# Optimization experiments

Hardware: AMD Instinct MI355X
Metric: run time of the kernel (lower is better)

The kernel has to match this reference:

```python
import jax, jax.numpy as jnp
import numpy as np

DIM = 512
NUM_HEADS = 8
HEAD_DIM = DIM // NUM_HEADS
FFN_DIM = 4 * DIM
EPS = 1e-6


def rmsnorm(x, w):
    rms = jnp.sqrt(jnp.mean(x * x, axis=-1, keepdims=True) + EPS)
    return x / rms * w


def setup_inputs() -> dict:
    key = jax.random.key(0)
    ks = jax.random.split(key, 8)
    B, T = 4, 2048
    x = jax.random.normal(ks[0], (B, T, DIM), dtype=jnp.float32)
    # Linear weights stored as [in, out] (transpose of torch layout)
    w_qkv = jax.random.normal(ks[1], (DIM, 3 * DIM), dtype=jnp.float32) * 0.02
    w_out = jax.random.normal(ks[2], (DIM, DIM), dtype=jnp.float32) * 0.02
    b_out = jnp.zeros((DIM,), dtype=jnp.float32)
    w1 = jax.random.normal(ks[3], (DIM, FFN_DIM), dtype=jnp.float32) * 0.02
    b1 = jnp.zeros((FFN_DIM,), dtype=jnp.float32)
    w2 = jax.random.normal(ks[4], (FFN_DIM, DIM), dtype=jnp.float32) * 0.02
    b2 = jnp.zeros((DIM,), dtype=jnp.float32)
    norm1_w = jnp.ones((DIM,), dtype=jnp.float32)
    norm2_w = jnp.ones((DIM,), dtype=jnp.float32)
    return {
        "x": x, "norm1_w": norm1_w, "norm2_w": norm2_w,
        "w_qkv": w_qkv, "w_out": w_out, "b_out": b_out,
        "w1": w1, "b1": b1, "w2": w2, "b2": b2,
        "context_size": 64,
    }


def reference(x, norm1_w, norm2_w, w_qkv, w_out, b_out, w1, b1, w2, b2, context_size):
    B, T, D = x.shape
    H, Hd = NUM_HEADS, HEAD_DIM
    # --- attention sublayer ---
    xn = rmsnorm(x, norm1_w)
    qkv = xn @ w_qkv                      # (B, T, 3D)
    q, k, v = jnp.split(qkv, 3, axis=-1)
    q = q.reshape(B, T, H, Hd).transpose(0, 2, 1, 3)  # (B, H, T, Hd)
    k = k.reshape(B, T, H, Hd).transpose(0, 2, 1, 3)
    v = v.reshape(B, T, H, Hd).transpose(0, 2, 1, 3)
    scale = Hd ** -0.5
    scores = jnp.einsum('bhqd,bhkd->bhqk', q, k) * scale  # (B, H, T, T)
    idx = jnp.arange(T)
    band = jnp.abs(idx[:, None] - idx[None, :]) <= context_size  # (T, T)
    scores = jnp.where(band[None, None], scores, -jnp.inf)
    attn = jax.nn.softmax(scores, axis=-1)
    out = jnp.einsum('bhqk,bhkd->bhqd', attn, v)  # (B, H, T, Hd)
    out = out.transpose(0, 2, 1, 3).reshape(B, T, D)
    out = out @ w_out + b_out
    x = x + out
    # --- FFN sublayer ---
    h = rmsnorm(x, norm2_w)
    h = jax.nn.gelu(h @ w1 + b1, approximate=False)
    x = x + (h @ w2 + b2)
    return x
```

## Files before the change

### kernel.cpp

```cpp
#include <hip/hip_runtime.h>
#include <cstdint>
#include <cstddef>

#define B_  4
#define T_  2048
#define D_  512
#define NH_ 8
#define HD_ 64
#define FF_ 2048
#define M_  (B_*T_)

typedef unsigned short u16;
typedef __attribute__((ext_vector_type(8))) unsigned short u16x8;
typedef __attribute__((ext_vector_type(8))) __bf16         bf16x8;
typedef __attribute__((ext_vector_type(4))) float          f32x4;

__device__ __forceinline__ u16 f2bf(float f) {
  unsigned u = __float_as_uint(f);
  u += 0x7FFF + ((u >> 16) & 1);
  return (u16)(u >> 16);
}
__device__ __forceinline__ float bf2f(u16 h) {
  return __uint_as_float((unsigned)h << 16);
}

__device__ __forceinline__ f32x4 mfma_bf16(u16x8 a, u16x8 b, f32x4 c) {
  return __builtin_amdgcn_mfma_f32_16x16x32_bf16(
      __builtin_bit_cast(bf16x8, a), __builtin_bit_cast(bf16x8, b), c, 0, 0, 0);
}

__device__ __forceinline__ void async16(const void* g, void* l) {
  __builtin_amdgcn_global_load_lds(
      (const __attribute__((address_space(1))) unsigned int*)g,
      (__attribute__((address_space(3))) unsigned int*)l, 16, 0, 0);
}

__device__ __forceinline__ float gelu_f(float v) {
  float ax = fabsf(v) * 0.70710678118f;
  float t = 1.0f / (1.0f + 0.3275911f * ax);
  float p = ((((1.061405429f * t - 1.453152027f) * t + 1.421413741f) * t
              - 0.284496736f) * t + 0.254829592f) * t;
  float e = __expf(-ax * ax);
  float er = 1.0f - p * e;
  float s = (v >= 0.0f) ? er : -er;
  return 0.5f * v * (1.0f + s);
}

__global__ __launch_bounds__(256) void prep_kernel(
    const float* __restrict__ i0, u16* __restrict__ o0,
    const float* __restrict__ i1, u16* __restrict__ o1,
    const float* __restrict__ i2, u16* __restrict__ o2,
    const float* __restrict__ i3, u16* __restrict__ o3,
    const float* __restrict__ x, const float* __restrict__ n1w,
    const float* __restrict__ n2w,
    float* __restrict__ inv, u16* __restrict__ xbf, float* __restrict__ ssz) {
  __shared__ float tile[32][33];
  const int bid = blockIdx.x, tid = threadIdx.x;
  if (bid < 3072) {
    const float* in; u16* out; const float* sc; int R, C, gx, lb;
    if (bid < 768)       { in = i0; out = o0; R = 512;  C = 1536; gx = 48; lb = bid;        sc = n1w; }
    else if (bid < 1024) { in = i1; out = o1; R = 512;  C = 512;  gx = 16; lb = bid - 768;  sc = nullptr; }
    else if (bid < 2048) { in = i2; out = o2; R = 512;  C = 2048; gx = 64; lb = bid - 1024; sc = n2w; }
    else                 { in = i3; out = o3; R = 2048; C = 512;  gx = 16; lb = bid - 2048; sc = nullptr; }
    int c0 = (lb % gx) * 32, r0 = (lb / gx) * 32;
    int tx = tid & 31, ty = tid >> 5;
#pragma unroll
    for (int i = 0; i < 4; i++)
      tile[ty + i * 8][tx] = in[(size_t)(r0 + ty + i * 8) * C + c0 + tx];
    __syncthreads();
    float s = sc ? sc[r0 + tx] : 1.0f;
#pragma unroll
    for (int i = 0; i < 4; i++)
      out[(size_t)(c0 + ty + i * 8) * R + r0 + tx] = f2bf(tile[tx][ty + i * 8] * s);
  } else if (bid < 5120) {
    int row  = (bid - 3072) * 4 + (tid >> 6);
    int lane = tid & 63;
    const float* xr = x + (size_t)row * D_ + lane * 8;
    float v[8];
    *(float4*)(v)     = *(const float4*)xr;
    *(float4*)(v + 4) = *(const float4*)(xr + 4);
    u16 rw[8];
#pragma unroll
    for (int e = 0; e < 8; e++) rw[e] = f2bf(v[e]);
    *(uint4*)(xbf + (size_t)row * D_ + lane * 8) = *(uint4*)rw;
    float ss = 0.f;
#pragma unroll
    for (int e = 0; e < 8; e++) ss += v[e] * v[e];
#pragma unroll
    for (int m = 1; m < 64; m <<= 1) ss += __shfl_xor(ss, m, 64);
    if (lane == 0) inv[row] = rsqrtf(ss * (1.0f / D_) + 1e-6f);
  } else {
    ssz[(bid - 5120) * 256 + tid] = 0.f;
  }
}

template <int BM, int BN, bool HAS_BIAS, int RES_MODE, bool DO_GELU,
          bool STORE_BF16, int SCALE_MODE, bool EMIT_SS>
__global__ __launch_bounds__(256) void gemm_kernel(
    const u16* __restrict__ A, const u16* __restrict__ Bt, void* __restrict__ Cv,
    const float* __restrict__ bias, const void* __restrict__ resv,
    const float* __restrict__ rowscale, float* __restrict__ ssout,
    int M, int N, int K) {
  constexpr int ACH = BM / 32;
  constexpr int BCH = BN / 32;
  constexpr int WM  = BM / 2, WN = BN / 2;
  constexpr int MI  = WM / 16, NJ = WN / 16;
  constexpr int EW  = BN + 4;
  constexpr int STG = (BM + BN) * 128;
  constexpr int EPB = 32 * EW * 4;
  constexpr int SMB = (2 * STG > EPB) ? 2 * STG : EPB;
  __shared__ __align__(16) char smem[SMB];
  const int tid = threadIdx.x;
  const int lane = tid & 63, w = tid >> 6;
  const int quad = lane >> 4, m16 = lane & 15;
  const int wm = w & 1, wn = w >> 1;

  const int nbx  = N / BN;
  const int wg   = blockIdx.x;
  const int xcd  = wg & 7, slot = wg >> 3;
  const int mper = (M / BM) >> 3;
  const int mloc = slot / nbx;
  const int nxp  = slot - mloc * nbx;
  const int m0 = (xcd * mper + mloc) * BM, n0 = nxp * BN;

  f32x4 acc[MI][NJ];
#pragma unroll
  for (int i = 0; i < MI; i++)
#pragma unroll
    for (int j = 0; j < NJ; j++) acc[i][j] = (f32x4){0.f, 0.f, 0.f, 0.f};

  const int srow = tid >> 3;
  const int scol = (((tid & 7) ^ (srow & 7))) * 8;
  const u16* Ag = A  + (size_t)(m0 + srow) * K + scol;
  const u16* Bg = Bt + (size_t)(n0 + srow) * K + scol;

  auto stage = [&](int buf, int kt) {
    char* base = smem + buf * STG;
#pragma unroll
    for (int c = 0; c < ACH; c++)
      async16(Ag + (size_t)c * 32 * K + kt, base + c * 4096 + tid * 16);
#pragma unroll
    for (int c = 0; c < BCH; c++)
      async16(Bg + (size_t)c * 32 * K + kt, base + BM * 128 + c * 4096 + tid * 16);
  };
  auto compute = [&](int buf) {
    const u16* lA = (const u16*)(smem + buf * STG);
    const u16* lB = (const u16*)(smem + buf * STG + BM * 128);
#pragma unroll
    for (int kk = 0; kk < 2; kk++) {
      const int sl = ((kk * 4 + quad) ^ (m16 & 7)) * 8;
      const u16* pa = lA + (wm * WM + m16) * 64 + sl;
      const u16* pb = lB + (wn * WN + m16) * 64 + sl;
      u16x8 af[MI], bfr[NJ];
#pragma unroll
      for (int i = 0; i < MI; i++) af[i] = *(const u16x8*)(pa + i * 1024);
#pragma unroll
      for (int j = 0; j < NJ; j++) bfr[j] = *(const u16x8*)(pb + j * 1024);
#pragma unroll
      for (int i = 0; i < MI; i++)
#pragma unroll
        for (int j = 0; j < NJ; j++)
          acc[i][j] = mfma_bf16(af[i], bfr[j], acc[i][j]);
    }
  };

  const int nk = K >> 6;
  stage(0, 0);
  for (int t = 0; t < nk; t++) {
    __syncthreads();
    if (t + 1 < nk) stage((t + 1) & 1, (t + 1) << 6);
    compute(t & 1);
  }

  float* eps = (float*)smem;
  constexpr int REPS = (32 * BN) / (256 * 8);
  float bv[REPS > 0 ? REPS : 1][8];
  if (HAS_BIAS) {
#pragma unroll
    for (int rep = 0; rep < REPS; rep++) {
      const int col = (BN == 128) ? ((tid & 15) * 8) : ((tid & 7) * 8);
      *(float4*)(bv[rep])     = *(const float4*)(bias + n0 + col);
      *(float4*)(bv[rep] + 4) = *(const float4*)(bias + n0 + col + 4);
    }
  }
#pragma unroll
  for (int i = 0; i < MI; i++) {
    __syncthreads();
#pragma unroll
    for (int j = 0; j < NJ; j++)
#pragma unroll
      for (int r = 0; r < 4; r++)
        eps[(wm * 16 + quad * 4 + r) * EW + wn * WN + j * 16 + m16] =
            acc[i][j][r];
    __syncthreads();
#pragma unroll
    for (int rep = 0; rep < REPS; rep++) {
      const int lr  = (BN == 128) ? (rep * 16 + (tid >> 4)) : (tid >> 3);
      const int col = (BN == 128) ? ((tid & 15) * 8) : ((tid & 7) * 8);
      const int rg  = m0 + (lr >> 4) * WM + i * 16 + (lr & 15);
      float v[8];
      *(float4*)(v)     = *(const float4*)(eps + lr * EW + col);
      *(float4*)(v + 4) = *(const float4*)(eps + lr * EW + col + 4);
      if (SCALE_MODE != 0) {
        float rs;
        if (SCALE_MODE == 1) rs = rowscale[rg];
        else                 rs = rsqrtf(rowscale[rg] * (1.0f / D_) + 1e-6f);
#pragma unroll
        for (int e = 0; e < 8; e++) v[e] *= rs;
      }
      if (HAS_BIAS) {
#pragma unroll
        for (int e = 0; e < 8; e++) v[e] += bv[rep][e];
      }
      if (DO_GELU) {
#pragma unroll
        for (int e = 0; e < 8; e++) v[e] = gelu_f(v[e]);
      }
      const size_t idx = (size_t)rg * N + n0 + col;
      if (RES_MODE == 1) {
        float4 r0 = *(const float4*)((const float*)resv + idx);
        float4 r1 = *(const float4*)((const float*)resv + idx + 4);
        v[0] += r0.x; v[1] += r0.y; v[2] += r0.z; v[3] += r0.w;
        v[4] += r1.x; v[5] += r1.y; v[6] += r1.z; v[7] += r1.w;
      } else if (RES_MODE == 2) {
        u16x8 rr = *(const u16x8*)((const u16*)resv + idx);
#pragma unroll
        for (int e = 0; e < 8; e++) v[e] += bf2f(rr[e]);
      }
      if (EMIT_SS) {
        float ps = 0.f;
#pragma unroll
        for (int e = 0; e < 8; e++) ps += v[e] * v[e];
        ps += __shfl_xor(ps, 1, 64);
        ps += __shfl_xor(ps, 2, 64);
        ps += __shfl_xor(ps, 4, 64);
        ps += __shfl_xor(ps, 8, 64);
        if ((tid & 15) == 0) atomicAdd(ssout + rg, ps);
      }
      if (STORE_BF16) {
        u16 o[8];
#pragma unroll
        for (int e = 0; e < 8; e++) o[e] = f2bf(v[e]);
        *(uint4*)((u16*)Cv + idx) = *(uint4*)o;
      } else {
        *(float4*)((float*)Cv + idx)     = *(float4*)(v);
        *(float4*)((float*)Cv + idx + 4) = *(float4*)(v + 4);
      }
    }
  }
}

#define VP_ 216
__global__ __launch_bounds__(256) void attn_kernel(const u16* __restrict__ qkv,
                                                   u16* __restrict__ out) {
  __shared__ __align__(16) char smem[26624 + 64 * VP_ * 2];
  u16* Ks = (u16*)smem;
  u16* Vt = (u16*)(smem + 26624);
  const int tid = threadIdx.x, lane = tid & 63, w = tid >> 6;
  const int quad = lane >> 4, m16 = lane & 15;
  const int qc = ((blockIdx.x & 7) << 2) | (blockIdx.x >> 3);
  const int q0 = qc * 64, h = blockIdx.y, b = blockIdx.z;
  const int kstart = q0 - 64;
  const u16* base = qkv + (size_t)b * T_ * 1536;

  for (int c = tid; c < 1664; c += 256) {
    int row = c >> 3, ch = c & 7;
    int j = kstart + row;
    j = j < 0 ? 0 : (j > T_ - 1 ? T_ - 1 : j);
    *(uint4*)(Ks + row * 64 + ((ch ^ (row & 7)) * 8)) =
        *(const uint4*)(base + (size_t)j * 1536 + 512 + h * 64 + ch * 8);
  }
  for (int c = tid; c < 1664; c += 256) {
    int row = c >> 3, cc = (c & 7) * 8;
    int j = kstart + row;
    j = j < 0 ? 0 : (j > T_ - 1 ? T_ - 1 : j);
    uint4 u = *(const uint4*)(base + (size_t)j * 1536 + 1024 + h * 64 + cc);
    u16 tmp[8];
    *(uint4*)tmp = u;
#pragma unroll
    for (int i = 0; i < 8; i++) Vt[(cc + i) * VP_ + row] = tmp[i];
  }
  const int qw = q0 + w * 16;
  const u16* qb = base + (size_t)(qw + m16) * 1536 + h * 64 + quad * 8;
  u16x8 a0 = *(const u16x8*)qb;
  u16x8 a1 = *(const u16x8*)(qb + 32);
  __syncthreads();

  float s[10][4];
#pragma unroll
  for (int t = 0; t < 10; t++) {
    int kt = (w + t) * 16;
    int kr = kt + m16, sw = kr & 7;
    u16x8 kb0 = *(const u16x8*)(Ks + kr * 64 + ((quad ^ sw) * 8));
    u16x8 kb1 = *(const u16x8*)(Ks + kr * 64 + (((4 + quad) ^ sw) * 8));
    f32x4 acc = {0.f, 0.f, 0.f, 0.f};
    acc = mfma_bf16(a0, kb0, acc);
    acc = mfma_bf16(a1, kb1, acc);
    int jab = kstart + kt + m16;
#pragma unroll
    for (int r = 0; r < 4; r++) {
      int q = qw + quad * 4 + r;
      int d = q - jab;
      bool valid = (jab >= 0) && (jab < T_) && (d <= 64) && (d >= -64);
      s[t][r] = valid ? acc[r] * 0.125f : -1e30f;
    }
  }
  float mx[4], sm[4];
#pragma unroll
  for (int r = 0; r < 4; r++) mx[r] = -1e30f;
#pragma unroll
  for (int t = 0; t < 10; t++)
#pragma unroll
    for (int r = 0; r < 4; r++) mx[r] = fmaxf(mx[r], s[t][r]);
#pragma unroll
  for (int r = 0; r < 4; r++) {
#pragma unroll
    for (int msk = 1; msk < 16; msk <<= 1)
      mx[r] = fmaxf(mx[r], __shfl_xor(mx[r], msk, 64));
    sm[r] = 0.f;
  }
#pragma unroll
  for (int t = 0; t < 10; t++)
#pragma unroll
    for (int r = 0; r < 4; r++) {
      float e = __expf(s[t][r] - mx[r]);
      s[t][r] = e; sm[r] += e;
    }
#pragma unroll
  for (int r = 0; r < 4; r++) {
#pragma unroll
    for (int msk = 1; msk < 16; msk <<= 1) sm[r] += __shfl_xor(sm[r], msk, 64);
    sm[r] = 1.0f / sm[r];
  }
  __syncthreads();
  u16* Ps = (u16*)smem + w * 2688;
#pragma unroll
  for (int t = 0; t < 10; t++)
#pragma unroll
    for (int r = 0; r < 4; r++)
      Ps[(quad * 4 + r) * 168 + t * 16 + m16] = f2bf(s[t][r] * sm[r]);
  __syncthreads();

  f32x4 o[4];
#pragma unroll
  for (int dt = 0; dt < 4; dt++) o[dt] = (f32x4){0.f, 0.f, 0.f, 0.f};
#pragma unroll
  for (int c5 = 0; c5 < 5; c5++) {
    u16x8 pa = *(const u16x8*)(Ps + m16 * 168 + c5 * 32 + quad * 8);
#pragma unroll
    for (int dt = 0; dt < 4; dt++) {
      u16x8 vb = *(const u16x8*)(Vt + (dt * 16 + m16) * VP_ + w * 16 + c5 * 32 + quad * 8);
      o[dt] = mfma_bf16(pa, vb, o[dt]);
    }
  }
#pragma unroll
  for (int dt = 0; dt < 4; dt++)
#pragma unroll
    for (int r = 0; r < 4; r++)
      out[(size_t)(b * T_ + qw + quad * 4 + r) * D_ + h * HD_ + dt * 16 + m16] =
          f2bf(o[dt][r]);
}

extern "C" void kernel_launch(void* const* d_in, const int* in_sizes, int n_in,
                              void* d_out, int out_size, void* d_ws, size_t ws_size,
                              hipStream_t stream) {
  (void)in_sizes; (void)n_in; (void)out_size; (void)ws_size;
  const float* x     = (const float*)d_in[0];
  const float* n1w   = (const float*)d_in[1];
  const float* n2w   = (const float*)d_in[2];
  const float* w_qkv = (const float*)d_in[3];
  const float* w_out = (const float*)d_in[4];
  const float* b_out = (const float*)d_in[5];
  const float* w1    = (const float*)d_in[6];
  const float* b1    = (const float*)d_in[7];
  const float* w2    = (const float*)d_in[8];
  const float* b2    = (const float*)d_in[9];
  float* out = (float*)d_out;
  char* ws = (char*)d_ws;

  u16* wqkvT  = (u16*)(ws + 0);
  u16* woutT  = (u16*)(ws + 1572864);
  u16* w1T    = (u16*)(ws + 2097152);
  u16* w2T    = (u16*)(ws + 4194304);
  float* inv  = (float*)(ws + 6291456);
  float* sums = (float*)(ws + 6324224);
  u16* qkv    = (u16*)(ws + 14680064);
  u16* attno  = (u16*)(ws + 39845888);
  u16* x1     = (u16*)(ws + 48234496);
  u16* xbf    = (u16*)(ws + 56623104);
  u16* hbuf   = qkv;

  prep_kernel<<<5152, 256, 0, stream>>>(
      w_qkv, wqkvT, w_out, woutT, w1, w1T, w2, w2T, x, n1w, n2w, inv, xbf, sums);

  gemm_kernel<64, 128, false, 0, false, true, 1, false>
      <<<dim3(12 * 128), 256, 0, stream>>>(
      xbf, wqkvT, (void*)qkv, nullptr, nullptr, inv, nullptr, M_, 3 * D_, D_);
  attn_kernel<<<dim3(32, 8, 4), 256, 0, stream>>>(qkv, attno);
  gemm_kernel<64, 128, true, 2, false, true, 0, true>
      <<<dim3(4 * 128), 256, 0, stream>>>(
      attno, woutT, (void*)x1, b_out, xbf, nullptr, sums, M_, D_, D_);
  gemm_kernel<128, 128, true, 0, true, true, 2, false>
      <<<dim3(16 * 64), 256, 0, stream>>>(
      x1, w1T, (void*)hbuf, b1, nullptr, sums, nullptr, M_, FF_, D_);
  gemm_kernel<64, 128, true, 2, false, false, 0, false>
      <<<dim3(4 * 128), 256, 0, stream>>>(
      hbuf, w2T, (void*)out, b2, x1, nullptr, nullptr, M_, D_, FF_);
}
```

Measured before the change: 203.5 us.

## Add 256x256-tile 8-wave GEMM kernel for QKV and FFN1 projections

Introduces a new GEMM kernel using 256x256 output tiles with 512 threads, 128KB dynamic LDS, double-buffered async global-to-LDS loads interleaved with MFMA quarters, XOR-swizzled LDS layout, XCD-aware block mapping, and s_setprio around MFMAs. It replaces the QKV and FFN-up GEMMs to raise data reuse per tile and overlap loads with compute. The cost is far fewer workgroups (192 and 256) on a 256-CU device, which may leave CUs idle or unbalanced, plus high register and LDS use per block.

```diff
diff --git a/kernel.cpp b/kernel.cpp
--- a/kernel.cpp
+++ b/kernel.cpp
@@ -91,6 +91,189 @@
     if (lane == 0) inv[row] = rsqrtf(ss * (1.0f / D_) + 1e-6f);
   } else {
     ssz[(bid - 5120) * 256 + tid] = 0.f;
+  }
+}
+
+template <bool HAS_BIAS, int SCALE_MODE, bool DO_GELU>
+__global__ __launch_bounds__(512) void gemm256_kernel(
+    const u16* __restrict__ A, const u16* __restrict__ Bt, u16* __restrict__ C,
+    const float* __restrict__ bias, const float* __restrict__ rowscale,
+    int M, int N, int K) {
+  extern __shared__ __align__(16) char dsmem[];
+  const int tid = threadIdx.x;
+  const int lane = tid & 63, w = tid >> 6;
+  const int quad = lane >> 4, m16 = lane & 15;
+  const int wm = w & 1, wn = w >> 1;
+  const int nbx = N >> 8;
+  const int wg  = blockIdx.x;
+  const int xcd = wg & 7, slot = wg >> 3;
+  const int mper = (M >> 8) >> 3;
+  const int mloc = slot / nbx, nxp = slot - mloc * nbx;
+  const int m0 = (xcd * mper + mloc) << 8, n0 = nxp << 8;
+
+  const int srow = tid >> 3;
+  const int scol = ((tid & 7) ^ (srow & 7)) * 8;
+  const u16* Ag = A  + (size_t)(m0 + srow) * K + scol;
+  const u16* Bg = Bt + (size_t)(n0 + srow) * K + scol;
+
+  auto stA = [&](int bsel, int kt, int half) {
+    char* d = dsmem + bsel * 32768 + half * 16384 + tid * 16;
+#pragma unroll
+    for (int c = 0; c < 2; c++)
+      async16(Ag + (size_t)(half * 128 + c * 64) * K + kt * 64, d + c * 8192);
+  };
+  auto stB = [&](int bsel, int kt, int half) {
+    char* d = dsmem + 65536 + bsel * 32768 + half * 16384 + tid * 16;
+#pragma unroll
+    for (int c = 0; c < 2; c++)
+      async16(Bg + (size_t)(half * 128 + c * 64) * K + kt * 64, d + c * 8192);
+  };
+
+  f32x4 acc[8][4];
+#pragma unroll
+  for (int i = 0; i < 8; i++)
+#pragma unroll
+    for (int j = 0; j < 4; j++) acc[i][j] = (f32x4){0.f, 0.f, 0.f, 0.f};
+
+  const int nk = K >> 6, nt = nk >> 1;
+  stA(0, 0, 0); stA(0, 0, 1); stB(0, 0, 0); stB(0, 0, 1);
+  stA(1, 1, 0); stA(1, 1, 1); stB(1, 1, 0); stB(1, 1, 1);
+  asm volatile("s_waitcnt vmcnt(8)" ::: "memory");
+  __builtin_amdgcn_s_barrier();
+
+  const u16* lA0 = (const u16*)(dsmem);
+  const u16* lA1 = (const u16*)(dsmem + 32768);
+  const u16* lB0 = (const u16*)(dsmem + 65536);
+  const u16* lB1 = (const u16*)(dsmem + 98304);
+
+  for (int t = 0; t < nt; ++t) {
+    const int t2 = t << 1;
+    const bool last = (t == nt - 1);
+    u16x8 bfr[4][2];
+#pragma unroll
+    for (int q = 0; q < 4; ++q) {
+      if (q == 0) {
+#pragma unroll
+        for (int j = 0; j < 4; ++j)
+#pragma unroll
+          for (int kk = 0; kk < 2; ++kk)
+            bfr[j][kk] = *(const u16x8*)(lB0 + (wn * 64 + j * 16 + m16) * 64 +
+                                         (((kk * 4 + quad) ^ (m16 & 7)) * 8));
+      }
+      u16x8 af[2][2];
+#pragma unroll
+      for (int s = 0; s < 2; ++s)
+#pragma unroll
+        for (int kk = 0; kk < 2; ++kk)
+          af[s][kk] = *(const u16x8*)(lA0 + (wm * 128 + (q * 2 + s) * 16 + m16) * 64 +
+                                      (((kk * 4 + quad) ^ (m16 & 7)) * 8));
+      if (q == 0 && t >= 1) stA(1, t2 + 1, 0);
+      if (q == 1) {
+        if (t >= 1) stA(1, t2 + 1, 1);
+        if (t2 + 2 < nk) stB(0, t2 + 2, 0);
+      }
+      if (q == 2 && t2 + 2 < nk) stB(0, t2 + 2, 1);
+      __builtin_amdgcn_s_barrier();
+      asm volatile("s_waitcnt lgkmcnt(0)" ::: "memory");
+      __builtin_amdgcn_s_setprio(1);
+#pragma unroll
+      for (int s = 0; s < 2; ++s)
+#pragma unroll
+        for (int kk = 0; kk < 2; ++kk)
+#pragma unroll
+          for (int j = 0; j < 4; ++j)
+            acc[q * 2 + s][j] = mfma_bf16(af[s][kk], bfr[j][kk], acc[q * 2 + s][j]);
+      __builtin_amdgcn_s_setprio(0);
+      if (q == 3) {
+        if (last) asm volatile("s_waitcnt vmcnt(0)" ::: "memory");
+        else      asm volatile("s_waitcnt vmcnt(4)" ::: "memory");
+      }
+      __builtin_amdgcn_s_barrier();
+    }
+#pragma unroll
+    for (int q = 0; q < 4; ++q) {
+      if (q == 0) {
+#pragma unroll
+        for (int j = 0; j < 4; ++j)
+#pragma unroll
+          for (int kk = 0; kk < 2; ++kk)
+            bfr[j][kk] = *(const u16x8*)(lB1 + (wn * 64 + j * 16 + m16) * 64 +
+                                         (((kk * 4 + quad) ^ (m16 & 7)) * 8));
+      }
+      u16x8 af[2][2];
+#pragma unroll
+      for (int s = 0; s < 2; ++s)
+#pragma unroll
+        for (int kk = 0; kk < 2; ++kk)
+          af[s][kk] = *(const u16x8*)(lA1 + (wm * 128 + (q * 2 + s) * 16 + m16) * 64 +
+                                      (((kk * 4 + quad) ^ (m16 & 7)) * 8));
+      if (q == 0 && t2 + 2 < nk) stA(0, t2 + 2, 0);
+      if (q == 1) {
+        if (t2 + 2 < nk) stA(0, t2 + 2, 1);
+        if (t2 + 3 < nk) stB(1, t2 + 3, 0);
+      }
+      if (q == 2 && t2 + 3 < nk) stB(1, t2 + 3, 1);
+      __builtin_amdgcn_s_barrier();
+      asm volatile("s_waitcnt lgkmcnt(0)" ::: "memory");
+      __builtin_amdgcn_s_setprio(1);
+#pragma unroll
+      for (int s = 0; s < 2; ++s)
+#pragma unroll
+        for (int kk = 0; kk < 2; ++kk)
+#pragma unroll
+          for (int j = 0; j < 4; ++j)
+            acc[q * 2 + s][j] = mfma_bf16(af[s][kk], bfr[j][kk], acc[q * 2 + s][j]);
+      __builtin_amdgcn_s_setprio(0);
+      if (q == 3 && !last)
+        asm volatile("s_waitcnt vmcnt(4)" ::: "memory");
+      __builtin_amdgcn_s_barrier();
+    }
+  }
+
+  __syncthreads();
+  float* eps = (float*)dsmem;
+  const int ecol = (tid & 31) * 8;
+  float bv[8];
+  if (HAS_BIAS) {
+    *(float4*)(bv)     = *(const float4*)(bias + n0 + ecol);
+    *(float4*)(bv + 4) = *(const float4*)(bias + n0 + ecol + 4);
+  }
+#pragma unroll
+  for (int i = 0; i < 8; ++i) {
+    __syncthreads();
+#pragma unroll
+    for (int j = 0; j < 4; ++j)
+#pragma unroll
+      for (int r = 0; r < 4; ++r)
+        eps[(wm * 16 + quad * 4 + r) * 260 + wn * 64 + j * 16 + m16] = acc[i][j][r];
+    __syncthreads();
+#pragma unroll
+    for (int rep = 0; rep < 2; ++rep) {
+      const int lr = rep * 16 + (tid >> 5);
+      const int rg = m0 + (lr >> 4) * 128 + i * 16 + (lr & 15);
+      float v[8];
+      *(float4*)(v)     = *(const float4*)(eps + lr * 260 + ecol);
+      *(float4*)(v + 4) = *(const float4*)(eps + lr * 260 + ecol + 4);
+      if (SCALE_MODE != 0) {
+        float rs;
+        if (SCALE_MODE == 1) rs = rowscale[rg];
+        else                 rs = rsqrtf(rowscale[rg] * (1.0f / D_) + 1e-6f);
+#pragma unroll
+        for (int e = 0; e < 8; e++) v[e] *= rs;
+      }
+      if (HAS_BIAS) {
+#pragma unroll
+        for (int e = 0; e < 8; e++) v[e] += bv[e];
+      }
+      if (DO_GELU) {
+#pragma unroll
+        for (int e = 0; e < 8; e++) v[e] = gelu_f(v[e]);
+      }
+      u16 o[8];
+#pragma unroll
+      for (int e = 0; e < 8; e++) o[e] = f2bf(v[e]);
+      *(uint4*)(C + (size_t)rg * N + n0 + ecol) = *(uint4*)o;
+    }
   }
 }
 
@@ -390,19 +573,26 @@
   u16* xbf    = (u16*)(ws + 56623104);
   u16* hbuf   = qkv;
 
+  static bool cfg = false;
+  if (!cfg) {
+    hipFuncSetAttribute((const void*)gemm256_kernel<false, 1, false>,
+                        hipFuncAttributeMaxDynamicSharedMemorySize, 131072);
+    hipFuncSetAttribute((const void*)gemm256_kernel<true, 2, true>,
+                        hipFuncAttributeMaxDynamicSharedMemorySize, 131072);
+    cfg = true;
+  }
+
   prep_kernel<<<5152, 256, 0, stream>>>(
       w_qkv, wqkvT, w_out, woutT, w1, w1T, w2, w2T, x, n1w, n2w, inv, xbf, sums);
 
-  gemm_kernel<64, 128, false, 0, false, true, 1, false>
-      <<<dim3(12 * 128), 256, 0, stream>>>(
-      xbf, wqkvT, (void*)qkv, nullptr, nullptr, inv, nullptr, M_, 3 * D_, D_);
+  gemm256_kernel<false, 1, false><<<192, 512, 131072, stream>>>(
+      xbf, wqkvT, qkv, nullptr, inv, M_, 3 * D_, D_);
   attn_kernel<<<dim3(32, 8, 4), 256, 0, stream>>>(qkv, attno);
   gemm_kernel<64, 128, true, 2, false, true, 0, true>
       <<<dim3(4 * 128), 256, 0, stream>>>(
       attno, woutT, (void*)x1, b_out, xbf, nullptr, sums, M_, D_, D_);
-  gemm_kernel<128, 128, true, 0, true, true, 2, false>
-      <<<dim3(16 * 64), 256, 0, stream>>>(
-      x1, w1T, (void*)hbuf, b1, nullptr, sums, nullptr, M_, FF_, D_);
+  gemm256_kernel<true, 2, true><<<256, 512, 131072, stream>>>(
+      x1, w1T, hbuf, b1, sums, M_, FF_, D_);
   gemm_kernel<64, 128, true, 2, false, false, 0, false>
       <<<dim3(4 * 128), 256, 0, stream>>>(
       hbuf, w2T, (void*)out, b2, x1, nullptr, nullptr, M_, D_, FF_);
```

After: 202.6 us. About the same (-0.4%).

## Replace atomic row sum-of-squares with partial buffers, async K loads, vmcnt pipelining

Applied to the files above, without the earlier changes.

The out-projection GEMM now writes per-N-tile partial sums of squares into four separate buffers, and the FFN1 epilogue sums them. This removes both the atomics and the zeroing blocks in the prep kernel. The GEMM main loop issues the next stage's loads before waiting with an explicit vmcnt, then uses raw barriers around compute, so global loads can overlap compute. Attention K tiles are now loaded with async global-to-LDS copies. The hardcoded vmcnt values rely on the stage() load count and on async16 being defined in the hidden code, which is a correctness risk.

```diff
diff --git a/kernel.cpp b/kernel.cpp
--- a/kernel.cpp
+++ b/kernel.cpp
@@ -53,7 +53,7 @@
     const float* __restrict__ i3, u16* __restrict__ o3,
     const float* __restrict__ x, const float* __restrict__ n1w,
     const float* __restrict__ n2w,
-    float* __restrict__ inv, u16* __restrict__ xbf, float* __restrict__ ssz) {
+    float* __restrict__ inv, u16* __restrict__ xbf) {
   __shared__ float tile[32][33];
   const int bid = blockIdx.x, tid = threadIdx.x;
   if (bid < 3072) {
@@ -72,7 +72,7 @@
 #pragma unroll
     for (int i = 0; i < 4; i++)
       out[(size_t)(c0 + ty + i * 8) * R + r0 + tx] = f2bf(tile[tx][ty + i * 8] * s);
-  } else if (bid < 5120) {
+  } else {
     int row  = (bid - 3072) * 4 + (tid >> 6);
     int lane = tid & 63;
     const float* xr = x + (size_t)row * D_ + lane * 8;
@@ -89,8 +89,6 @@
 #pragma unroll
     for (int m = 1; m < 64; m <<= 1) ss += __shfl_xor(ss, m, 64);
     if (lane == 0) inv[row] = rsqrtf(ss * (1.0f / D_) + 1e-6f);
-  } else {
-    ssz[(bid - 5120) * 256 + tid] = 0.f;
   }
 }
 
@@ -103,12 +101,14 @@
     int M, int N, int K) {
   constexpr int ACH = BM / 32;
   constexpr int BCH = BN / 32;
+  constexpr int NLD = ACH + BCH;
   constexpr int WM  = BM / 2, WN = BN / 2;
   constexpr int MI  = WM / 16, NJ = WN / 16;
   constexpr int EW  = BN + 4;
   constexpr int STG = (BM + BN) * 128;
   constexpr int EPB = 32 * EW * 4;
   constexpr int SMB = (2 * STG > EPB) ? 2 * STG : EPB;
+  static_assert(NLD == 6 || NLD == 8, "vmcnt literal covers 6 or 8");
   __shared__ __align__(16) char smem[SMB];
   const int tid = threadIdx.x;
   const int lane = tid & 63, w = tid >> 6;
@@ -167,9 +167,18 @@
   const int nk = K >> 6;
   stage(0, 0);
   for (int t = 0; t < nk; t++) {
-    __syncthreads();
-    if (t + 1 < nk) stage((t + 1) & 1, (t + 1) << 6);
+    if (t + 1 < nk) {
+      stage((t + 1) & 1, (t + 1) << 6);
+      if constexpr (NLD == 6)
+        asm volatile("s_waitcnt vmcnt(6)" ::: "memory");
+      else
+        asm volatile("s_waitcnt vmcnt(8)" ::: "memory");
+    } else {
+      asm volatile("s_waitcnt vmcnt(0)" ::: "memory");
+    }
+    __builtin_amdgcn_s_barrier();
     compute(t & 1);
+    __builtin_amdgcn_s_barrier();
   }
 
   float* eps = (float*)smem;
@@ -203,8 +212,13 @@
       *(float4*)(v + 4) = *(const float4*)(eps + lr * EW + col + 4);
       if (SCALE_MODE != 0) {
         float rs;
-        if (SCALE_MODE == 1) rs = rowscale[rg];
-        else                 rs = rsqrtf(rowscale[rg] * (1.0f / D_) + 1e-6f);
+        if (SCALE_MODE == 1)      rs = rowscale[rg];
+        else if (SCALE_MODE == 2) rs = rsqrtf(rowscale[rg] * (1.0f / D_) + 1e-6f);
+        else {
+          float s4 = rowscale[rg] + rowscale[M_ + rg] +
+                     rowscale[2 * M_ + rg] + rowscale[3 * M_ + rg];
+          rs = rsqrtf(s4 * (1.0f / D_) + 1e-6f);
+        }
 #pragma unroll
         for (int e = 0; e < 8; e++) v[e] *= rs;
       }
@@ -235,7 +249,7 @@
         ps += __shfl_xor(ps, 2, 64);
         ps += __shfl_xor(ps, 4, 64);
         ps += __shfl_xor(ps, 8, 64);
-        if ((tid & 15) == 0) atomicAdd(ssout + rg, ps);
+        if ((tid & 15) == 0) ssout[(size_t)nxp * M + rg] = ps;
       }
       if (STORE_BF16) {
         u16 o[8];
@@ -263,12 +277,22 @@
   const int kstart = q0 - 64;
   const u16* base = qkv + (size_t)b * T_ * 1536;
 
-  for (int c = tid; c < 1664; c += 256) {
-    int row = c >> 3, ch = c & 7;
+#pragma unroll
+  for (int r6 = 0; r6 < 6; r6++) {
+    int c = r6 * 256 + tid;
+    int row = c >> 3;
     int j = kstart + row;
     j = j < 0 ? 0 : (j > T_ - 1 ? T_ - 1 : j);
-    *(uint4*)(Ks + row * 64 + ((ch ^ (row & 7)) * 8)) =
-        *(const uint4*)(base + (size_t)j * 1536 + 512 + h * 64 + ch * 8);
+    int srcch = ((c & 7) ^ (row & 7)) * 8;
+    async16(base + (size_t)j * 1536 + 512 + h * 64 + srcch, smem + c * 16);
+  }
+  if (tid < 128) {
+    int c = 1536 + tid;
+    int row = c >> 3;
+    int j = kstart + row;
+    j = j < 0 ? 0 : (j > T_ - 1 ? T_ - 1 : j);
+    int srcch = ((c & 7) ^ (row & 7)) * 8;
+    async16(base + (size_t)j * 1536 + 512 + h * 64 + srcch, smem + c * 16);
   }
   for (int c = tid; c < 1664; c += 256) {
     int row = c >> 3, cc = (c & 7) * 8;
@@ -383,15 +407,15 @@
   u16* w1T    = (u16*)(ws + 2097152);
   u16* w2T    = (u16*)(ws + 4194304);
   float* inv  = (float*)(ws + 6291456);
-  float* sums = (float*)(ws + 6324224);
+  float* sums4= (float*)(ws + 6324224);
   u16* qkv    = (u16*)(ws + 14680064);
   u16* attno  = (u16*)(ws + 39845888);
   u16* x1     = (u16*)(ws + 48234496);
   u16* xbf    = (u16*)(ws + 56623104);
   u16* hbuf   = qkv;
 
-  prep_kernel<<<5152, 256, 0, stream>>>(
-      w_qkv, wqkvT, w_out, woutT, w1, w1T, w2, w2T, x, n1w, n2w, inv, xbf, sums);
+  prep_kernel<<<5120, 256, 0, stream>>>(
+      w_qkv, wqkvT, w_out, woutT, w1, w1T, w2, w2T, x, n1w, n2w, inv, xbf);
 
   gemm_kernel<64, 128, false, 0, false, true, 1, false>
       <<<dim3(12 * 128), 256, 0, stream>>>(
@@ -399,10 +423,10 @@
   attn_kernel<<<dim3(32, 8, 4), 256, 0, stream>>>(qkv, attno);
   gemm_kernel<64, 128, true, 2, false, true, 0, true>
       <<<dim3(4 * 128), 256, 0, stream>>>(
-      attno, woutT, (void*)x1, b_out, xbf, nullptr, sums, M_, D_, D_);
-  gemm_kernel<128, 128, true, 0, true, true, 2, false>
+      attno, woutT, (void*)x1, b_out, xbf, nullptr, sums4, M_, D_, D_);
+  gemm_kernel<128, 128, true, 0, true, true, 3, false>
       <<<dim3(16 * 64), 256, 0, stream>>>(
-      x1, w1T, (void*)hbuf, b1, nullptr, sums, nullptr, M_, FF_, D_);
+      x1, w1T, (void*)hbuf, b1, nullptr, sums4, nullptr, M_, FF_, D_);
   gemm_kernel<64, 128, true, 2, false, false, 0, false>
       <<<dim3(4 * 128), 256, 0, stream>>>(
       hbuf, w2T, (void*)out, b2, x1, nullptr, nullptr, M_, D_, FF_);
```

Result: faster. 198.5 us (-2.4%).
